# Kernel tuning notes

Measured on AMD Instinct MI355X. Metric: run time of the kernel, lower is better.

The kernel has to match this reference:

```python
import jax, jax.numpy as jnp
import numpy as np

KH, KW = 3, 3          # kernel_size
STRIDE, PAD, DIL = 1, 1, 1
DG = 1                 # deformable_groups


def setup_inputs() -> dict:
    key = jax.random.key(0)
    k1, k2 = jax.random.split(key)
    x = jax.random.normal(k1, (4, 64, 128, 128), dtype=jnp.float32)
    # offset layout: [B, 2*DG*KH*KW, Ho, Wo], pairs are (dy, dx) per tap
    offset = jax.random.normal(k2, (4, 2 * DG * KH * KW, 128, 128), dtype=jnp.float32)
    return {"input": x, "offset": offset}


def _deform_unfold(x, offset):
    B, C, H, W = x.shape
    Ho = (H + 2 * PAD - DIL * (KH - 1) - 1) // STRIDE + 1
    Wo = (W + 2 * PAD - DIL * (KW - 1) - 1) // STRIDE + 1
    K = KH * KW
    Cg = C // DG

    off = offset.reshape(B, DG, K, 2, Ho, Wo)
    oy, ox = off[:, :, :, 0], off[:, :, :, 1]          # [B,DG,K,Ho,Wo]

    # tap displacements within the kernel window
    ky = (jnp.repeat(jnp.arange(KH), KW) * DIL).astype(x.dtype)  # [K]
    kx = (jnp.tile(jnp.arange(KW), KH) * DIL).astype(x.dtype)    # [K]
    gy = (jnp.arange(Ho) * STRIDE - PAD).astype(x.dtype)         # [Ho]
    gx = (jnp.arange(Wo) * STRIDE - PAD).astype(x.dtype)         # [Wo]

    # fractional sampling coordinates  [B,DG,K,Ho,Wo]
    py = oy + gy[None, None, None, :, None] + ky[None, None, :, None, None]
    px = ox + gx[None, None, None, None, :] + kx[None, None, :, None, None]

    y0 = jnp.floor(py)
    x0 = jnp.floor(px)
    wy1 = py - y0
    wx1 = px - x0
    wy0 = 1.0 - wy1
    wx0 = 1.0 - wx1
    y0i = y0.astype(jnp.int32)
    x0i = x0.astype(jnp.int32)

    x_flat = x.reshape(B, DG, Cg, H * W)

    def corner(yi, xi, w):
        valid = ((yi >= 0) & (yi < H) & (xi >= 0) & (xi < W)).astype(x.dtype)
        idx = jnp.clip(yi, 0, H - 1) * W + jnp.clip(xi, 0, W - 1)   # [B,DG,K,Ho,Wo]
        idxf = idx.reshape(B, DG, K * Ho * Wo)
        # gather: xf [Cg,HW], ix [N] -> [Cg,N]; vmapped over B and DG
        g = jax.vmap(jax.vmap(lambda xf, ix: xf[:, ix]))(x_flat, idxf)
        g = g.reshape(B, DG, Cg, K, Ho, Wo)
        return g * (w * valid)[:, :, None]        # broadcast over Cg

    out = (corner(y0i, x0i, wy0 * wx0)
           + corner(y0i, x0i + 1, wy0 * wx1)
           + corner(y0i + 1, x0i, wy1 * wx0)
           + corner(y0i + 1, x0i + 1, wy1 * wx1))   # [B,DG,Cg,K,Ho,Wo]

    # im2col layout: channel-major, tap-minor -> [B, C*K, Ho*Wo]
    return out.reshape(B, C * K, Ho * Wo)


def reference(input, offset):
    return _deform_unfold(input, offset)
```

## Files before the change

### kernel.cpp

```cpp
#include <hip/hip_runtime.h>


#define BB 4
#define CC 64
#define HH 128
#define WW 128
#define KK 9
#define HW (HH * WW)
#define NR 16
#define CG 8
#define NG (CC / CG)
#define TPB 256

#define LDS_BARRIER()                                         \
    do {                                                      \
        asm volatile("s_waitcnt lgkmcnt(0)" ::: "memory");    \
        __builtin_amdgcn_s_barrier();                         \
        asm volatile("" ::: "memory");                        \
    } while (0)

__global__ __launch_bounds__(TPB) void deform_unfold_lds(
    const float* __restrict__ x, const float* __restrict__ off,
    float* __restrict__ out)
{
    __shared__ float2 tile[2][NR * WW];
    __shared__ int anyfall;

    const int tid = threadIdx.x;
    const int bid = blockIdx.x;
    const int g = bid & (NG - 1);
    const int t = (bid >> 3) & 63;
    const int b = bid >> 9;

    const int s  = t * TPB + tid;
    const int wo = s & (WW - 1);
    const int ho = s >> 7;
    const int r0 = min(max(2 * t - 6, 0), HH - NR);

    const int c0g = g * CG;
    const float* xb = x + ((size_t)b * CC + c0g) * HW;
    float* ob = out + (((size_t)b * CC + c0g) * KK) * HW + s;

    float2 ca[4], cb[4];
    {
        const float2* A2 = (const float2*)(xb + (size_t)r0 * WW);
        const float2* B2 = (const float2*)(xb + HW + (size_t)r0 * WW);
        #pragma unroll
        for (int j = 0; j < 4; ++j) { ca[j] = A2[tid + 256 * j]; cb[j] = B2[tid + 256 * j]; }
    }

    if (tid == 0) anyfall = 0;
    __syncthreads();

    float u0[KK], u1[KK], t0w[KK], t1w[KK];
    int aAB[KK];
    int myfall = 0;
    #pragma unroll
    for (int k = 0; k < KK; ++k) {
        int ky = k / 3, kx = k - ky * 3;
        float oy = off[(((size_t)b * (2 * KK)) + 2 * k) * HW + s];
        float ox = off[(((size_t)b * (2 * KK)) + 2 * k + 1) * HW + s];
        float py = oy + (float)(ho - 1 + ky);
        float px = ox + (float)(wo - 1 + kx);
        float y0f = floorf(py), x0f = floorf(px);
        float wy1 = py - y0f, wx1 = px - x0f;
        float wy0 = 1.f - wy1, wx0 = 1.f - wx1;
        int y0 = (int)y0f, x0 = (int)x0f;
        int y1 = y0 + 1, x1 = x0 + 1;
        bool vy0 = (y0 >= 0) && (y0 < HH), vy1 = (y1 >= 0) && (y1 < HH);
        bool vx0 = (x0 >= 0) && (x0 < WW), vx1 = (x1 >= 0) && (x1 < WW);
        int y0c = min(max(y0, 0), HH - 1), y1c = min(max(y1, 0), HH - 1);
        int xa  = min(max(x0, 0), WW - 2);
        int i0  = min(max(x0, 0), WW - 1) - xa;
        int i1  = min(max(x1, 0), WW - 1) - xa;
        float w00 = wy0 * wx0 * ((vy0 && vx0) ? 1.f : 0.f);
        float w01 = wy0 * wx1 * ((vy0 && vx1) ? 1.f : 0.f);
        float w10 = wy1 * wx0 * ((vy1 && vx0) ? 1.f : 0.f);
        float w11 = wy1 * wx1 * ((vy1 && vx1) ? 1.f : 0.f);
        u0[k]  = (i0 == 0 ? w00 : 0.f) + (i1 == 0 ? w01 : 0.f);
        u1[k]  = (i0 == 1 ? w00 : 0.f) + (i1 == 1 ? w01 : 0.f);
        t0w[k] = (i0 == 0 ? w10 : 0.f) + (i1 == 0 ? w11 : 0.f);
        t1w[k] = (i0 == 1 ? w10 : 0.f) + (i1 == 1 ? w11 : 0.f);
        int rA = y0c - r0, rB = y1c - r0;
        myfall |= ((unsigned)rA >= NR) | ((unsigned)rB >= NR);
        rA = min(max(rA, 0), NR - 1);
        rB = min(max(rB, 0), NR - 1);
        aAB[k] = (rA * WW + xa) | ((rB * WW + xa) << 16);
    }
    if (myfall) atomicOr(&anyfall, 1);
    __syncthreads();
    const bool fall = (anyfall != 0);

    if (!fall) {
        int cur = 0;
        #pragma unroll
        for (int cp = 0; cp < CG / 2; ++cp) {
            float2 na[4], nb[4];
            if (cp + 1 < CG / 2) {
                const float2* A2 = (const float2*)(xb + (size_t)(2 * cp + 2) * HW + (size_t)r0 * WW);
                const float2* B2 = (const float2*)(xb + (size_t)(2 * cp + 3) * HW + (size_t)r0 * WW);
                #pragma unroll
                for (int j = 0; j < 4; ++j) { na[j] = A2[tid + 256 * j]; nb[j] = B2[tid + 256 * j]; }
            }
            float4* wt = (float4*)tile[cur];
            #pragma unroll
            for (int j = 0; j < 4; ++j)
                wt[tid + 256 * j] = make_float4(ca[j].x, cb[j].x, ca[j].y, cb[j].y);
            LDS_BARRIER();
            const float2* tl = tile[cur];
            float* o = ob + (size_t)(2 * cp) * KK * HW;
            #pragma unroll
            for (int k = 0; k < KK; ++k) {
                int aA = aAB[k] & 0xffff, aB = aAB[k] >> 16;
                float2 p00 = tl[aA], p01 = tl[aA + 1];
                float2 p10 = tl[aB], p11 = tl[aB + 1];
                float vx_ = p00.x * u0[k] + p01.x * u1[k] + p10.x * t0w[k] + p11.x * t1w[k];
                float vy_ = p00.y * u0[k] + p01.y * u1[k] + p10.y * t0w[k] + p11.y * t1w[k];
                __builtin_nontemporal_store(vx_, o + (size_t)k * HW);
                __builtin_nontemporal_store(vy_, o + (size_t)(KK + k) * HW);
            }
            #pragma unroll
            for (int j = 0; j < 4; ++j) { ca[j] = na[j]; cb[j] = nb[j]; }
            cur ^= 1;
        }
    } else {
        #pragma unroll 1
        for (int k = 0; k < KK; ++k) {
            int ky = k / 3, kx = k - ky * 3;
            float oy = off[(((size_t)b * (2 * KK)) + 2 * k) * HW + s];
            float ox = off[(((size_t)b * (2 * KK)) + 2 * k + 1) * HW + s];
            float py = oy + (float)(ho - 1 + ky);
            float px = ox + (float)(wo - 1 + kx);
            float y0f = floorf(py), x0f = floorf(px);
            float wy1 = py - y0f, wx1 = px - x0f;
            float wy0 = 1.f - wy1, wx0 = 1.f - wx1;
            int y0 = (int)y0f, x0 = (int)x0f;
            int y1 = y0 + 1, x1 = x0 + 1;
            bool vy0 = (y0 >= 0) && (y0 < HH), vy1 = (y1 >= 0) && (y1 < HH);
            bool vx0 = (x0 >= 0) && (x0 < WW), vx1 = (x1 >= 0) && (x1 < WW);
            int y0c = min(max(y0, 0), HH - 1), y1c = min(max(y1, 0), HH - 1);
            int x0c = min(max(x0, 0), WW - 1), x1c = min(max(x1, 0), WW - 1);
            float w00 = wy0 * wx0 * ((vy0 && vx0) ? 1.f : 0.f);
            float w01 = wy0 * wx1 * ((vy0 && vx1) ? 1.f : 0.f);
            float w10 = wy1 * wx0 * ((vy1 && vx0) ? 1.f : 0.f);
            float w11 = wy1 * wx1 * ((vy1 && vx1) ? 1.f : 0.f);
            int o00 = y0c * WW + x0c, o01 = y0c * WW + x1c;
            int o10 = y1c * WW + x0c, o11 = y1c * WW + x1c;
            #pragma unroll 1
            for (int c = 0; c < CG; ++c) {
                const float* xc = xb + (size_t)c * HW;
                (ob + (size_t)c * KK * HW)[(size_t)k * HW] =
                    xc[o00] * w00 + xc[o01] * w01 + xc[o10] * w10 + xc[o11] * w11;
            }
        }
    }
}

extern "C" void kernel_launch(void* const* d_in, const int* in_sizes, int n_in,
                              void* d_out, int out_size, void* d_ws, size_t ws_size,
                              hipStream_t stream) {
    const float* x   = (const float*)d_in[0];
    const float* off = (const float*)d_in[1];
    float* out = (float*)d_out;

    int blocks = BB * 64 * NG;
    deform_unfold_lds<<<blocks, TPB, 0, stream>>>(x, off, out);
}
```

Baseline: 38.93 us.

## Single-buffer padded LDS tile, ballot-based fallback flag, and batch offset loads

Replaces the double-buffered LDS tile with a single buffer that has a 130-element row pitch, halving LDS use and reducing bank conflicts on the gather reads. The next channel pair is now loaded directly into the existing registers after the current data is stored to LDS, which drops the separate prefetch registers. A bare barrier at the top of each iteration guards reuse of the single buffer. The shared atomic fallback flag is replaced by per-wave ballots combined through LDS, and all offset loads are issued up front so they overlap with the first tile load. The cost is an extra barrier per channel pair and less overlap between the global prefetch and LDS writes.

```diff
diff --git a/kernel.cpp b/kernel.cpp
--- a/kernel.cpp
+++ b/kernel.cpp
@@ -8,6 +8,7 @@
 #define KK 9
 #define HW (HH * WW)
 #define NR 16
+#define PITCH 130
 #define CG 8
 #define NG (CC / CG)
 #define TPB 256
@@ -19,12 +20,19 @@
         asm volatile("" ::: "memory");                        \
     } while (0)
 
+#define BARE_BARRIER()                                        \
+    do {                                                      \
+        asm volatile("" ::: "memory");                        \
+        __builtin_amdgcn_s_barrier();                         \
+        asm volatile("" ::: "memory");                        \
+    } while (0)
+
 __global__ __launch_bounds__(TPB) void deform_unfold_lds(
     const float* __restrict__ x, const float* __restrict__ off,
     float* __restrict__ out)
 {
-    __shared__ float2 tile[2][NR * WW];
-    __shared__ int anyfall;
+    __shared__ float2 tile[NR * PITCH];
+    __shared__ int wf[TPB / 64];
 
     const int tid = threadIdx.x;
     const int bid = blockIdx.x;
@@ -41,6 +49,15 @@
     const float* xb = x + ((size_t)b * CC + c0g) * HW;
     float* ob = out + (((size_t)b * CC + c0g) * KK) * HW + s;
 
+    float oyv[KK], oxv[KK];
+    {
+        const float* offb = off + ((size_t)b * (2 * KK)) * HW + s;
+        #pragma unroll
+        for (int k = 0; k < KK; ++k) {
+            oyv[k] = offb[(size_t)(2 * k) * HW];
+            oxv[k] = offb[(size_t)(2 * k + 1) * HW];
+        }
+    }
     float2 ca[4], cb[4];
     {
         const float2* A2 = (const float2*)(xb + (size_t)r0 * WW);
@@ -49,19 +66,14 @@
         for (int j = 0; j < 4; ++j) { ca[j] = A2[tid + 256 * j]; cb[j] = B2[tid + 256 * j]; }
     }
 
-    if (tid == 0) anyfall = 0;
-    __syncthreads();
-
     float u0[KK], u1[KK], t0w[KK], t1w[KK];
     int aAB[KK];
     int myfall = 0;
     #pragma unroll
     for (int k = 0; k < KK; ++k) {
         int ky = k / 3, kx = k - ky * 3;
-        float oy = off[(((size_t)b * (2 * KK)) + 2 * k) * HW + s];
-        float ox = off[(((size_t)b * (2 * KK)) + 2 * k + 1) * HW + s];
-        float py = oy + (float)(ho - 1 + ky);
-        float px = ox + (float)(wo - 1 + kx);
+        float py = oyv[k] + (float)(ho - 1 + ky);
+        float px = oxv[k] + (float)(wo - 1 + kx);
         float y0f = floorf(py), x0f = floorf(px);
         float wy1 = py - y0f, wx1 = px - x0f;
         float wy0 = 1.f - wy1, wx0 = 1.f - wx1;
@@ -85,29 +97,32 @@
         myfall |= ((unsigned)rA >= NR) | ((unsigned)rB >= NR);
         rA = min(max(rA, 0), NR - 1);
         rB = min(max(rB, 0), NR - 1);
-        aAB[k] = (rA * WW + xa) | ((rB * WW + xa) << 16);
+        aAB[k] = (rA * PITCH + xa) | ((rB * PITCH + xa) << 16);
     }
-    if (myfall) atomicOr(&anyfall, 1);
-    __syncthreads();
-    const bool fall = (anyfall != 0);
+    unsigned long long bal = __ballot(myfall != 0);
+    if ((tid & 63) == 0) wf[tid >> 6] = (bal != 0) ? 1 : 0;
+    LDS_BARRIER();
+    const bool fall = (wf[0] | wf[1] | wf[2] | wf[3]) != 0;
 
     if (!fall) {
-        int cur = 0;
         #pragma unroll
         for (int cp = 0; cp < CG / 2; ++cp) {
-            float2 na[4], nb[4];
+            if (cp > 0) BARE_BARRIER();
+            float4* wt = (float4*)tile;
+            #pragma unroll
+            for (int j = 0; j < 4; ++j) {
+                int id = tid + 256 * j;
+                wt[(id >> 6) * (PITCH / 2) + (id & 63)] =
+                    make_float4(ca[j].x, cb[j].x, ca[j].y, cb[j].y);
+            }
             if (cp + 1 < CG / 2) {
                 const float2* A2 = (const float2*)(xb + (size_t)(2 * cp + 2) * HW + (size_t)r0 * WW);
                 const float2* B2 = (const float2*)(xb + (size_t)(2 * cp + 3) * HW + (size_t)r0 * WW);
                 #pragma unroll
-                for (int j = 0; j < 4; ++j) { na[j] = A2[tid + 256 * j]; nb[j] = B2[tid + 256 * j]; }
+                for (int j = 0; j < 4; ++j) { ca[j] = A2[tid + 256 * j]; cb[j] = B2[tid + 256 * j]; }
             }
-            float4* wt = (float4*)tile[cur];
-            #pragma unroll
-            for (int j = 0; j < 4; ++j)
-                wt[tid + 256 * j] = make_float4(ca[j].x, cb[j].x, ca[j].y, cb[j].y);
             LDS_BARRIER();
-            const float2* tl = tile[cur];
+            const float2* tl = tile;
             float* o = ob + (size_t)(2 * cp) * KK * HW;
             #pragma unroll
             for (int k = 0; k < KK; ++k) {
@@ -119,9 +134,6 @@
                 __builtin_nontemporal_store(vx_, o + (size_t)k * HW);
                 __builtin_nontemporal_store(vy_, o + (size_t)(KK + k) * HW);
             }
-            #pragma unroll
-            for (int j = 0; j < 4; ++j) { ca[j] = na[j]; cb[j] = nb[j]; }
-            cur ^= 1;
         }
     } else {
         #pragma unroll 1
```

Result: no change. 38.81 us (-0.3%).
